# Kernel tuning notes

Hardware: AMD Instinct MI355X
Metric: run time of the kernel (lower is better)

Reference implementation:

```python
import jax, jax.numpy as jnp
import numpy as np


def setup_inputs() -> dict:
    key = jax.random.key(0)
    k1, k2 = jax.random.split(key)
    B, TOTAL_BITS, H, W = 16, 64, 128, 128
    C_OUT, N_BITS = 64, 4
    # binary bit-plane input, values in {0, 1}
    x = (jax.random.uniform(k1, (B, TOTAL_BITS, H, W)) < 0.5).astype(jnp.float32)
    # random bit-selection map: which input bit feeds each (out_channel, bit_pos)
    rp_map = jax.random.randint(k2, (C_OUT, N_BITS), 0, TOTAL_BITS)
    return {"x": x, "rp_map": rp_map}


def reference(x, rp_map):
    # bit_select_mode path of RPLayer.forward:
    #   gather n_bits_per_out random bits per output channel, then
    #   bit-pack with power-of-two weights (MAC-free projection).
    B, TB, H, W = x.shape
    C, nb = rp_map.shape
    # [B, TB, H, W] -> [B*H*W, TB]
    x_flat = x.transpose(0, 2, 3, 1).reshape(B * H * W, TB)
    # gather: [B*H*W, C, nb]  (fancy-index along bit axis, no expand needed)
    gathered = x_flat[:, rp_map]
    # power-of-two pack weights [1, 2, 4, 8, ...]
    pack_w = 2.0 ** jnp.arange(nb, dtype=x.dtype)
    packed = jnp.einsum('ncb,b->nc', gathered, pack_w)  # [B*H*W, C]
    # [B, H, W, C] -> [B, C, H, W]
    return packed.reshape(B, H, W, C).transpose(0, 3, 1, 2)
```

## Files before the change

kernel.cpp:

```cpp
#include <hip/hip_runtime.h>
#include <cstdint>
#include <cstddef>

constexpr int Bn = 16;
constexpr int TBn = 64;
constexpr int Hn = 128;
constexpr int Wn = 128;
constexpr int Cn = 64;
constexpr int HW = Hn * Wn;
constexpr int TOTAL_PIX = Bn * HW;

__global__ __launch_bounds__(256) void rp_pack_pixel(
    const float* __restrict__ x,
    const int* __restrict__ rp,
    float* __restrict__ out)
{
    __shared__ int4 s_rp[Cn];
    if (threadIdx.x < Cn) {
        s_rp[threadIdx.x] = reinterpret_cast<const int4*>(rp)[threadIdx.x];
    }
    __syncthreads();

    const int p = blockIdx.x * blockDim.x + threadIdx.x;
    const int b = p >> 14;
    const int pix = p & (HW - 1);

    const float* xb = x + (size_t)b * TBn * HW + pix;
    float* ob = out + (size_t)b * Cn * HW + pix;

    uint64_t m = 0;
    #pragma unroll
    for (int t = 0; t < TBn; ++t) {
        const unsigned u = __float_as_uint(xb[(size_t)t * HW]);
        m |= (uint64_t)((u >> 23) & 1u) << t;
    }

    #pragma unroll 8
    for (int c = 0; c < Cn; ++c) {
        const int4 r = s_rp[c];
        const unsigned v = (unsigned)((m >> (unsigned)r.x) & 1ull)
                         | ((unsigned)((m >> (unsigned)r.y) & 1ull) << 1)
                         | ((unsigned)((m >> (unsigned)r.z) & 1ull) << 2)
                         | ((unsigned)((m >> (unsigned)r.w) & 1ull) << 3);
        ob[(size_t)c * HW] = (float)v;
    }
}

extern "C" void kernel_launch(void* const* d_in, const int* in_sizes, int n_in,
                              void* d_out, int out_size, void* d_ws, size_t ws_size,
                              hipStream_t stream) {
    const float* x = (const float*)d_in[0];
    const int* rp = (const int*)d_in[1];
    float* out = (float*)d_out;

    constexpr int BLOCK = 256;
    constexpr int GRID = TOTAL_PIX / BLOCK;
    rp_pack_pixel<<<GRID, BLOCK, 0, stream>>>(x, rp, out);
}
```

Before: 27.35 us.

## Vectorize pixel loads with float4 and split output channels across blocks

```diff
diff --git a/kernel.cpp b/kernel.cpp
--- a/kernel.cpp
+++ b/kernel.cpp
@@ -9,8 +9,13 @@
 constexpr int Cn = 64;
 constexpr int HW = Hn * Wn;
 constexpr int TOTAL_PIX = Bn * HW;
+constexpr int GROUPS = TOTAL_PIX / 4;
+constexpr int GROUPS_PER_BLOCK = 256;
+constexpr int PBLKS = GROUPS / GROUPS_PER_BLOCK;
+constexpr int CH_SPLIT = 4;
+constexpr int CH_PER = Cn / CH_SPLIT;
 
-__global__ __launch_bounds__(256) void rp_pack_pixel(
+__global__ __launch_bounds__(256) void rp_pack_f4(
     const float* __restrict__ x,
     const int* __restrict__ rp,
     float* __restrict__ out)
@@ -21,28 +26,55 @@
     }
     __syncthreads();
 
-    const int p = blockIdx.x * blockDim.x + threadIdx.x;
-    const int b = p >> 14;
-    const int pix = p & (HW - 1);
+    const int bid = blockIdx.x;
+    const int q = bid & 3;
+    const int pblk = bid >> 2;
+
+    const int g = pblk * GROUPS_PER_BLOCK + threadIdx.x;
+    const int b = g >> 12;
+    const int pix = (g & 4095) << 2;
 
     const float* xb = x + (size_t)b * TBn * HW + pix;
-    float* ob = out + (size_t)b * Cn * HW + pix;
+    float* ob = out + (size_t)b * Cn * HW + (size_t)(q * CH_PER) * HW + pix;
 
-    uint64_t m = 0;
+    uint64_t m0 = 0, m1 = 0, m2 = 0, m3 = 0;
     #pragma unroll
     for (int t = 0; t < TBn; ++t) {
-        const unsigned u = __float_as_uint(xb[(size_t)t * HW]);
-        m |= (uint64_t)((u >> 23) & 1u) << t;
+        const float4 v = *reinterpret_cast<const float4*>(xb + (size_t)t * HW);
+        m0 |= (uint64_t)((__float_as_uint(v.x) >> 23) & 1u) << t;
+        m1 |= (uint64_t)((__float_as_uint(v.y) >> 23) & 1u) << t;
+        m2 |= (uint64_t)((__float_as_uint(v.z) >> 23) & 1u) << t;
+        m3 |= (uint64_t)((__float_as_uint(v.w) >> 23) & 1u) << t;
     }
 
-    #pragma unroll 8
-    for (int c = 0; c < Cn; ++c) {
-        const int4 r = s_rp[c];
-        const unsigned v = (unsigned)((m >> (unsigned)r.x) & 1ull)
-                         | ((unsigned)((m >> (unsigned)r.y) & 1ull) << 1)
-                         | ((unsigned)((m >> (unsigned)r.z) & 1ull) << 2)
-                         | ((unsigned)((m >> (unsigned)r.w) & 1ull) << 3);
-        ob[(size_t)c * HW] = (float)v;
+    const int c0 = q * CH_PER;
+    #pragma unroll
+    for (int ci = 0; ci < CH_PER; ++ci) {
+        const int4 r = s_rp[c0 + ci];
+        const unsigned i0 = (unsigned)r.x;
+        const unsigned i1 = (unsigned)r.y;
+        const unsigned i2 = (unsigned)r.z;
+        const unsigned i3 = (unsigned)r.w;
+
+        float4 o;
+        o.x = (float)((unsigned)((m0 >> i0) & 1ull)
+                    | ((unsigned)((m0 >> i1) & 1ull) << 1)
+                    | ((unsigned)((m0 >> i2) & 1ull) << 2)
+                    | ((unsigned)((m0 >> i3) & 1ull) << 3));
+        o.y = (float)((unsigned)((m1 >> i0) & 1ull)
+                    | ((unsigned)((m1 >> i1) & 1ull) << 1)
+                    | ((unsigned)((m1 >> i2) & 1ull) << 2)
+                    | ((unsigned)((m1 >> i3) & 1ull) << 3));
+        o.z = (float)((unsigned)((m2 >> i0) & 1ull)
+                    | ((unsigned)((m2 >> i1) & 1ull) << 1)
+                    | ((unsigned)((m2 >> i2) & 1ull) << 2)
+                    | ((unsigned)((m2 >> i3) & 1ull) << 3));
+        o.w = (float)((unsigned)((m3 >> i0) & 1ull)
+                    | ((unsigned)((m3 >> i1) & 1ull) << 1)
+                    | ((unsigned)((m3 >> i2) & 1ull) << 2)
+                    | ((unsigned)((m3 >> i3) & 1ull) << 3));
+
+        *reinterpret_cast<float4*>(ob + (size_t)ci * HW) = o;
     }
 }
 
@@ -54,6 +86,6 @@
     float* out = (float*)d_out;
 
     constexpr int BLOCK = 256;
-    constexpr int GRID = TOTAL_PIX / BLOCK;
-    rp_pack_pixel<<<GRID, BLOCK, 0, stream>>>(x, rp, out);
+    constexpr int GRID = PBLKS * CH_SPLIT;
+    rp_pack_f4<<<GRID, BLOCK, 0, stream>>>(x, rp, out);
 }
```

New measurement: 62.20 us. 2.27x slower.
